# Kernel optimization log

Hardware: AMD Instinct MI355X
Metric: run time of the kernel (lower is better)

## Reference

```python
import jax, jax.numpy as jnp
import numpy as np

H = 1024   # hidden size
L = 3      # num layers
D_IN = 2048  # input size (= 2*H so every layer has the same input width)


def _bigru_layer(x_proj, W_hh, b_hh, h0):
    """Run one bidirectional GRU layer over time.
    x_proj: (T, 2, B, 3H)  input projections, time already reversed for dir=1
    W_hh:   (2, 3H, H)     hidden-to-hidden weights per direction
    b_hh:   (2, 3H)        hidden-to-hidden bias per direction
    h0:     (2, B, H)      initial hidden state per direction
    returns (T, 2, B, H)   hidden states per step (dir=1 still time-reversed)
    """
    def step(h, xp):
        # torch GRU convention: gates ordered [r, z, n]; reset gate multiplies
        # the hidden-side candidate term (W_hn h + b_hn).
        hh = jnp.einsum('dbh,dgh->dbg', h, W_hh) + b_hh[:, None, :]  # (2,B,3H)
        xr, xz, xn = jnp.split(xp, 3, axis=-1)
        hr, hz, hn = jnp.split(hh, 3, axis=-1)
        r = jax.nn.sigmoid(xr + hr)
        z = jax.nn.sigmoid(xz + hz)
        n = jnp.tanh(xn + r * hn)
        h_new = (1.0 - z) * n + z * h
        return h_new, h_new

    _, outs = jax.lax.scan(step, h0, x_proj)
    return outs


def setup_inputs() -> dict:
    key = jax.random.key(0)
    ks = jax.random.split(key, 8)
    T, B = 256, 32
    k = 1.0 / np.sqrt(H)  # torch default GRU init scale
    x = jax.random.normal(ks[0], (T, B, D_IN), dtype=jnp.float32)
    h0 = jax.random.normal(ks[1], (L * 2, B, H), dtype=jnp.float32)
    W_ih = jax.random.uniform(ks[2], (L, 2, 3 * H, D_IN), jnp.float32, -k, k)
    W_hh = jax.random.uniform(ks[3], (L, 2, 3 * H, H), jnp.float32, -k, k)
    b_ih = jax.random.uniform(ks[4], (L, 2, 3 * H), jnp.float32, -k, k)
    b_hh = jax.random.uniform(ks[5], (L, 2, 3 * H), jnp.float32, -k, k)
    return {"x": x, "h0": h0, "W_ih": W_ih, "W_hh": W_hh, "b_ih": b_ih, "b_hh": b_hh}


def reference(x, h0, W_ih, W_hh, b_ih, b_hh):
    T, B, _ = x.shape
    h0 = h0.reshape(L, 2, B, H)
    layer_input = x
    for l in range(L):
        # precompute input projections for both directions: (T, 2, B, 3H)
        xp = jnp.einsum('tbi,dgi->tdbg', layer_input, W_ih[l]) + b_ih[l][None, :, None, :]
        # reverse time for the backward direction
        xp = jnp.stack([xp[:, 0], xp[::-1, 1]], axis=1)
        outs = _bigru_layer(xp, W_hh[l], b_hh[l], h0[l])  # (T,2,B,H)
        out_f = outs[:, 0]
        out_b = outs[::-1, 1]  # un-reverse backward outputs
        layer_input = jnp.concatenate([out_f, out_b], axis=-1)  # (T,B,2H)
    return layer_input
```

## Files before the change

kernel.cpp:

```cpp
#include <hip/hip_runtime.h>
#include <hip/hip_bf16.h>
#include <stdint.h>

#define T_STEPS 256
#define BATCH   32
#define HID     1024
#define KDIM    2048
#define NDIM    6144
#define MDIM    8192

typedef __attribute__((ext_vector_type(8))) short bfrag;
typedef __attribute__((ext_vector_type(4))) float ffrag;

__device__ inline unsigned short f2bf(float f) {
  __hip_bfloat16 h = __float2bfloat16(f);
  unsigned short u;
  __builtin_memcpy(&u, &h, 2);
  return u;
}

__device__ inline void gld_lds16(const void* g, void* l) {
  __builtin_amdgcn_global_load_lds(
      (const __attribute__((address_space(1))) void*)g,
      (__attribute__((address_space(3))) void*)l,
      16, 0, 0);
}

__global__ __launch_bounds__(256) void f32_to_bf16_k(
    const float* __restrict__ src, unsigned short* __restrict__ dst, int n4) {
  int i = blockIdx.x * 256 + threadIdx.x;
  if (i >= n4) return;
  float4 v = ((const float4*)src)[i];
  ushort4 o;
  o.x = f2bf(v.x); o.y = f2bf(v.y); o.z = f2bf(v.z); o.w = f2bf(v.w);
  ((ushort4*)dst)[i] = o;
}

__global__ __launch_bounds__(256) void gemm_xp(
    const unsigned short* __restrict__ A,
    const unsigned short* __restrict__ Bw,
    const float* __restrict__ bias,
    float* __restrict__ C) {
  __shared__ __align__(16) unsigned short Asl[128 * 32];
  __shared__ __align__(16) unsigned short Bsl[128 * 32];
  const int tid  = threadIdx.x;
  const int wave = tid >> 6;
  const int lane = tid & 63;
  const int quad = lane >> 4;
  const int lm   = lane & 15;
  const int m0 = blockIdx.x * 128;
  const int n0 = blockIdx.y * 128;
  const int wm = (wave & 1) * 64;
  const int wn = (wave >> 1) * 64;

  ffrag acc[4][4];
#pragma unroll
  for (int a = 0; a < 4; a++)
#pragma unroll
    for (int b = 0; b < 4; b++) {
      ffrag z = {0.0f, 0.0f, 0.0f, 0.0f};
      acc[a][b] = z;
    }

  const int r = tid >> 2;
  const int c = tid & 3;
  const unsigned short* Ag0 = A  + (size_t)(m0 + r) * KDIM + c * 8;
  const unsigned short* Ag1 = Ag0 + (size_t)64 * KDIM;
  const unsigned short* Bg0 = Bw + (size_t)(n0 + r) * KDIM + c * 8;
  const unsigned short* Bg1 = Bg0 + (size_t)64 * KDIM;
  char* Al = (char*)Asl + wave * 1024;
  char* Bl = (char*)Bsl + wave * 1024;

  for (int kk = 0; kk < KDIM; kk += 32) {
    __syncthreads();
    gld_lds16(Ag0 + kk, Al);
    gld_lds16(Ag1 + kk, Al + 4096);
    gld_lds16(Bg0 + kk, Bl);
    gld_lds16(Bg1 + kk, Bl + 4096);
    __syncthreads();

    bfrag af[4], bf[4];
#pragma unroll
    for (int mt = 0; mt < 4; mt++)
      af[mt] = *(const bfrag*)((const char*)Asl + (wm + mt * 16 + lm) * 64 + quad * 16);
#pragma unroll
    for (int nt = 0; nt < 4; nt++)
      bf[nt] = *(const bfrag*)((const char*)Bsl + (wn + nt * 16 + lm) * 64 + quad * 16);
#pragma unroll
    for (int mt = 0; mt < 4; mt++)
#pragma unroll
      for (int nt = 0; nt < 4; nt++)
        acc[mt][nt] = __builtin_amdgcn_mfma_f32_16x16x32_bf16(
            af[mt], bf[nt], acc[mt][nt], 0, 0, 0);
  }

#pragma unroll
  for (int mt = 0; mt < 4; mt++) {
#pragma unroll
    for (int nt = 0; nt < 4; nt++) {
      int mrow = m0 + wm + mt * 16 + quad * 4;
      int ncol = n0 + wn + nt * 16 + lm;
      float bi = bias[ncol];
#pragma unroll
      for (int i = 0; i < 4; i++)
        C[(size_t)(mrow + i) * NDIM + ncol] = acc[mt][nt][i] + bi;
    }
  }
}

__device__ inline void gbar(unsigned* cnt, unsigned target) {
  __syncthreads();
  if (threadIdx.x == 0) {
    __hip_atomic_fetch_add(cnt, 1u, __ATOMIC_RELEASE, __HIP_MEMORY_SCOPE_AGENT);
    while (__hip_atomic_load(cnt, __ATOMIC_RELAXED, __HIP_MEMORY_SCOPE_AGENT) < target)
      __builtin_amdgcn_s_sleep(1);
    (void)__hip_atomic_load(cnt, __ATOMIC_ACQUIRE, __HIP_MEMORY_SCOPE_AGENT);
  }
  __syncthreads();
}

__global__ __launch_bounds__(384, 1) void gru_scan(
    const float* __restrict__ xp,
    const unsigned short* __restrict__ Wbf,
    const float* __restrict__ bhh,
    const float* __restrict__ h0,
    unsigned short* __restrict__ hbA, unsigned short* __restrict__ hbB,
    unsigned* __restrict__ bar,
    unsigned short* __restrict__ out_bf,
    float* __restrict__ out_f32) {
  __shared__ float gbuf[3][32][17];
  __shared__ float hloc[32][16];

  const int blk  = blockIdx.x;
  const int d    = blk >> 6;
  const int j0   = (blk & 63) * 16;
  const int tid  = threadIdx.x;
  const int wave = tid / 64;
  const int lane = tid & 63;
  const int quad = lane >> 4;
  const int lm   = lane & 15;
  const int g    = wave >> 1;
  const int mt   = wave & 1;

  const unsigned short* wrow =
      Wbf + ((size_t)(d * 3072 + g * 1024 + j0 + lm)) * HID + quad * 8;
  bfrag wreg[32];
#pragma unroll
  for (int kk = 0; kk < 32; kk++)
    wreg[kk] = *(const bfrag*)(wrow + kk * 32);

  const int arow_off = (d * 32 + mt * 16 + lm) * HID + quad * 8;

  for (int o = tid; o < 512; o += 384) {
    int b = o >> 4, j = o & 15;
    float v = h0[(d * 32 + b) * HID + j0 + j];
    hloc[b][j] = v;
    hbA[(d * 32 + b) * HID + j0 + j] = f2bf(v);
  }

  float bh_r[2], bh_z[2], bh_n[2];
#pragma unroll
  for (int u = 0; u < 2; u++) {
    int o = tid + u * 384;
    if (o < 512) {
      int jg = j0 + (o & 15);
      bh_r[u] = bhh[d * 3072 + jg];
      bh_z[u] = bhh[d * 3072 + 1024 + jg];
      bh_n[u] = bhh[d * 3072 + 2048 + jg];
    }
  }

  unsigned bt = 128;
  gbar(bar, bt);

  const unsigned short* hb_prev = hbA;
  unsigned short* hb_next = hbB;

  for (int s = 0; s < T_STEPS; s++) {
    const int t = d ? (T_STEPS - 1 - s) : s;

    float pxr[2], pxz[2], pxn[2];
#pragma unroll
    for (int u = 0; u < 2; u++) {
      int o = tid + u * 384;
      if (o < 512) {
        int b = o >> 4, jg = j0 + (o & 15);
        const float* xrow = xp + ((size_t)t * BATCH + b) * NDIM + d * 3072;
        pxr[u] = __builtin_nontemporal_load(xrow + jg);
        pxz[u] = __builtin_nontemporal_load(xrow + 1024 + jg);
        pxn[u] = __builtin_nontemporal_load(xrow + 2048 + jg);
      }
    }

    ffrag acc0 = {0.0f, 0.0f, 0.0f, 0.0f};
    ffrag acc1 = {0.0f, 0.0f, 0.0f, 0.0f};
    const unsigned short* ap = hb_prev + arow_off;
#pragma unroll
    for (int kk = 0; kk < 32; kk += 2) {
      bfrag a0 = *(const bfrag*)(ap + kk * 32);
      bfrag a1 = *(const bfrag*)(ap + kk * 32 + 32);
      acc0 = __builtin_amdgcn_mfma_f32_16x16x32_bf16(a0, wreg[kk],     acc0, 0, 0, 0);
      acc1 = __builtin_amdgcn_mfma_f32_16x16x32_bf16(a1, wreg[kk + 1], acc1, 0, 0, 0);
    }

    __syncthreads();
#pragma unroll
    for (int i = 0; i < 4; i++)
      gbuf[g][mt * 16 + quad * 4 + i][lm] = acc0[i] + acc1[i];
    __syncthreads();

#pragma unroll
    for (int u = 0; u < 2; u++) {
      int o = tid + u * 384;
      if (o < 512) {
        int b = o >> 4, j = o & 15;
        int jg = j0 + j;
        float hr = gbuf[0][b][j] + bh_r[u];
        float hz = gbuf[1][b][j] + bh_z[u];
        float hn = gbuf[2][b][j] + bh_n[u];
        float rr = 1.0f / (1.0f + __expf(-(pxr[u] + hr)));
        float zz = 1.0f / (1.0f + __expf(-(pxz[u] + hz)));
        float nn = tanhf(pxn[u] + rr * hn);
        float hp = hloc[b][j];
        float hv = (1.0f - zz) * nn + zz * hp;
        hloc[b][j] = hv;
        unsigned short hvb = f2bf(hv);
        hb_next[(d * 32 + b) * HID + jg] = hvb;
        size_t oi = ((size_t)t * BATCH + b) * 2048 + d * HID + jg;
        if (out_bf) __builtin_nontemporal_store(hvb, &out_bf[oi]);
        else        __builtin_nontemporal_store(hv, &out_f32[oi]);
      }
    }

    bt += 128;
    gbar(bar, bt);

    const unsigned short* tb = hb_prev;
    hb_prev = hb_next;
    hb_next = (unsigned short*)tb;
  }
}

extern "C" void kernel_launch(void* const* d_in, const int* in_sizes, int n_in,
                              void* d_out, int out_size, void* d_ws, size_t ws_size,
                              hipStream_t stream) {
  const float* x    = (const float*)d_in[0];
  const float* h0   = (const float*)d_in[1];
  const float* W_ih = (const float*)d_in[2];
  const float* W_hh = (const float*)d_in[3];
  const float* b_ih = (const float*)d_in[4];
  const float* b_hh = (const float*)d_in[5];
  float* out = (float*)d_out;

  char* w = (char*)d_ws;
  float* xp = (float*)w;                    w += (size_t)MDIM * NDIM * 4;
  unsigned short* act = (unsigned short*)w; w += (size_t)MDIM * KDIM * 2;
  unsigned short* Wub = (unsigned short*)w; w += (size_t)2 * 3072 * KDIM * 2;
  unsigned short* hbA = (unsigned short*)w; w += (size_t)2 * BATCH * HID * 2;
  unsigned short* hbB = (unsigned short*)w; w += (size_t)2 * BATCH * HID * 2;
  unsigned* bar = (unsigned*)w;             w += 256;

  hipMemsetAsync(bar, 0, 3 * sizeof(unsigned), stream);

  f32_to_bf16_k<<<16384, 256, 0, stream>>>(x, act, MDIM * KDIM / 4);

  for (int l = 0; l < 3; l++) {
    f32_to_bf16_k<<<12288, 256, 0, stream>>>(
        W_ih + (size_t)l * 2 * 3072 * KDIM, Wub, 2 * 3072 * KDIM / 4);
    dim3 gg(MDIM / 128, NDIM / 128);
    gemm_xp<<<gg, 256, 0, stream>>>(act, Wub, b_ih + l * NDIM, xp);
    f32_to_bf16_k<<<6144, 256, 0, stream>>>(
        W_hh + (size_t)l * 2 * 3072 * HID, Wub, 2 * 3072 * HID / 4);

    const float* xp_c = xp;
    const unsigned short* Wbf_c = Wub;
    const float* bhl = b_hh + l * NDIM;
    const float* h0l = h0 + (size_t)l * 2 * BATCH * HID;
    unsigned short* hbA_ = hbA; unsigned short* hbB_ = hbB;
    unsigned* bar_ = bar + l;
    unsigned short* dst_bf = (l == 2) ? nullptr : act;
    float* dst_f32 = (l == 2) ? out : nullptr;
    void* args[] = {
        (void*)&xp_c, (void*)&Wbf_c, (void*)&bhl, (void*)&h0l,
        (void*)&hbA_, (void*)&hbB_, (void*)&bar_,
        (void*)&dst_bf, (void*)&dst_f32,
    };
    hipLaunchCooperativeKernel((void*)gru_scan, dim3(128), dim3(384),
                               args, 0, stream);
  }
}
```

Measured before the change: 11.61 ms.

## Split grid barrier per direction, relax atomics, prefetch next-step projections

The single 128-block grid barrier becomes two independent 64-block barriers, one per direction, using relaxed atomics split into arrive and wait phases. The next step's input projections are loaded between arrive and wait so that load hides behind the barrier. Hidden-state reads and writes now go through relaxed agent-scope atomics, and each thread handles two packed elements in the gate stage. The recurrent weights are no longer held in registers and are reloaded from memory every step, which adds cache traffic. The removed release/acquire fences also risk memory-ordering problems.

```diff
diff --git a/kernel.cpp b/kernel.cpp
--- a/kernel.cpp
+++ b/kernel.cpp
@@ -11,6 +11,11 @@
 
 typedef __attribute__((ext_vector_type(8))) short bfrag;
 typedef __attribute__((ext_vector_type(4))) float ffrag;
+
+typedef union {
+  bfrag f;
+  unsigned long long q[2];
+} abuf;
 
 __device__ inline unsigned short f2bf(float f) {
   __hip_bfloat16 h = __float2bfloat16(f);
@@ -108,17 +113,6 @@
   }
 }
 
-__device__ inline void gbar(unsigned* cnt, unsigned target) {
-  __syncthreads();
-  if (threadIdx.x == 0) {
-    __hip_atomic_fetch_add(cnt, 1u, __ATOMIC_RELEASE, __HIP_MEMORY_SCOPE_AGENT);
-    while (__hip_atomic_load(cnt, __ATOMIC_RELAXED, __HIP_MEMORY_SCOPE_AGENT) < target)
-      __builtin_amdgcn_s_sleep(1);
-    (void)__hip_atomic_load(cnt, __ATOMIC_ACQUIRE, __HIP_MEMORY_SCOPE_AGENT);
-  }
-  __syncthreads();
-}
-
 __global__ __launch_bounds__(384, 1) void gru_scan(
     const float* __restrict__ xp,
     const unsigned short* __restrict__ Wbf,
@@ -135,43 +129,60 @@
   const int d    = blk >> 6;
   const int j0   = (blk & 63) * 16;
   const int tid  = threadIdx.x;
-  const int wave = tid / 64;
   const int lane = tid & 63;
   const int quad = lane >> 4;
   const int lm   = lane & 15;
-  const int g    = wave >> 1;
-  const int mt   = wave & 1;
+  const int g    = (tid / 64) >> 1;
+  const int mt   = (tid / 64) & 1;
+
+  unsigned* mybar = bar + d * 64;
+
+  const int gb  = tid >> 3;
+  const int gj  = (tid & 7) * 2;
+  const bool gact = (tid < 256);
+
+  if (gact) {
+    float v0 = h0[(d * 32 + gb) * HID + j0 + gj];
+    float v1 = h0[(d * 32 + gb) * HID + j0 + gj + 1];
+    hloc[gb][gj]     = v0;
+    hloc[gb][gj + 1] = v1;
+    unsigned pk = (unsigned)f2bf(v0) | ((unsigned)f2bf(v1) << 16);
+    __hip_atomic_store((unsigned*)&hbA[(d * 32 + gb) * HID + j0 + gj], pk,
+                       __ATOMIC_RELAXED, __HIP_MEMORY_SCOPE_AGENT);
+  }
+
+  float bh_r0 = 0, bh_r1 = 0, bh_z0 = 0, bh_z1 = 0, bh_n0 = 0, bh_n1 = 0;
+  if (gact) {
+    int jg = j0 + gj;
+    bh_r0 = bhh[d * 3072 + jg];        bh_r1 = bhh[d * 3072 + jg + 1];
+    bh_z0 = bhh[d * 3072 + 1024 + jg]; bh_z1 = bhh[d * 3072 + 1024 + jg + 1];
+    bh_n0 = bhh[d * 3072 + 2048 + jg]; bh_n1 = bhh[d * 3072 + 2048 + jg + 1];
+  }
 
   const unsigned short* wrow =
       Wbf + ((size_t)(d * 3072 + g * 1024 + j0 + lm)) * HID + quad * 8;
-  bfrag wreg[32];
-#pragma unroll
-  for (int kk = 0; kk < 32; kk++)
-    wreg[kk] = *(const bfrag*)(wrow + kk * 32);
-
   const int arow_off = (d * 32 + mt * 16 + lm) * HID + quad * 8;
 
-  for (int o = tid; o < 512; o += 384) {
-    int b = o >> 4, j = o & 15;
-    float v = h0[(d * 32 + b) * HID + j0 + j];
-    hloc[b][j] = v;
-    hbA[(d * 32 + b) * HID + j0 + j] = f2bf(v);
-  }
-
-  float bh_r[2], bh_z[2], bh_n[2];
-#pragma unroll
-  for (int u = 0; u < 2; u++) {
-    int o = tid + u * 384;
-    if (o < 512) {
-      int jg = j0 + (o & 15);
-      bh_r[u] = bhh[d * 3072 + jg];
-      bh_z[u] = bhh[d * 3072 + 1024 + jg];
-      bh_n[u] = bhh[d * 3072 + 2048 + jg];
-    }
-  }
-
-  unsigned bt = 128;
-  gbar(bar, bt);
+  unsigned bt = 64;
+  __syncthreads();
+  if (tid == 0)
+    __hip_atomic_fetch_add(mybar, 1u, __ATOMIC_RELAXED, __HIP_MEMORY_SCOPE_AGENT);
+
+  float2 pxr, pxz, pxn;
+  {
+    const int t0 = d ? (T_STEPS - 1) : 0;
+    const float* xrow = xp + ((size_t)t0 * BATCH + gb) * NDIM + d * 3072 + j0 + gj;
+    if (gact) {
+      pxr = *(const float2*)(xrow);
+      pxz = *(const float2*)(xrow + 1024);
+      pxn = *(const float2*)(xrow + 2048);
+    }
+  }
+  if (tid == 0) {
+    while (__hip_atomic_load(mybar, __ATOMIC_RELAXED, __HIP_MEMORY_SCOPE_AGENT) < bt)
+      __builtin_amdgcn_s_sleep(1);
+  }
+  __syncthreads();
 
   const unsigned short* hb_prev = hbA;
   unsigned short* hb_next = hbB;
@@ -179,28 +190,24 @@
   for (int s = 0; s < T_STEPS; s++) {
     const int t = d ? (T_STEPS - 1 - s) : s;
 
-    float pxr[2], pxz[2], pxn[2];
-#pragma unroll
-    for (int u = 0; u < 2; u++) {
-      int o = tid + u * 384;
-      if (o < 512) {
-        int b = o >> 4, jg = j0 + (o & 15);
-        const float* xrow = xp + ((size_t)t * BATCH + b) * NDIM + d * 3072;
-        pxr[u] = __builtin_nontemporal_load(xrow + jg);
-        pxz[u] = __builtin_nontemporal_load(xrow + 1024 + jg);
-        pxn[u] = __builtin_nontemporal_load(xrow + 2048 + jg);
-      }
+    abuf a[32];
+    const unsigned short* ap = hb_prev + arow_off;
+#pragma unroll
+    for (int kk = 0; kk < 32; kk++) {
+      a[kk].q[0] = __hip_atomic_load((const unsigned long long*)(ap + kk * 32),
+                                     __ATOMIC_RELAXED, __HIP_MEMORY_SCOPE_AGENT);
+      a[kk].q[1] = __hip_atomic_load((const unsigned long long*)(ap + kk * 32 + 4),
+                                     __ATOMIC_RELAXED, __HIP_MEMORY_SCOPE_AGENT);
     }
 
     ffrag acc0 = {0.0f, 0.0f, 0.0f, 0.0f};
     ffrag acc1 = {0.0f, 0.0f, 0.0f, 0.0f};
-    const unsigned short* ap = hb_prev + arow_off;
 #pragma unroll
     for (int kk = 0; kk < 32; kk += 2) {
-      bfrag a0 = *(const bfrag*)(ap + kk * 32);
-      bfrag a1 = *(const bfrag*)(ap + kk * 32 + 32);
-      acc0 = __builtin_amdgcn_mfma_f32_16x16x32_bf16(a0, wreg[kk],     acc0, 0, 0, 0);
-      acc1 = __builtin_amdgcn_mfma_f32_16x16x32_bf16(a1, wreg[kk + 1], acc1, 0, 0, 0);
+      bfrag w0 = *(const bfrag*)(wrow + kk * 32);
+      bfrag w1 = *(const bfrag*)(wrow + (kk + 1) * 32);
+      acc0 = __builtin_amdgcn_mfma_f32_16x16x32_bf16(a[kk].f,     w0, acc0, 0, 0, 0);
+      acc1 = __builtin_amdgcn_mfma_f32_16x16x32_bf16(a[kk + 1].f, w1, acc1, 0, 0, 0);
     }
 
     __syncthreads();
@@ -209,31 +216,53 @@
       gbuf[g][mt * 16 + quad * 4 + i][lm] = acc0[i] + acc1[i];
     __syncthreads();
 
-#pragma unroll
-    for (int u = 0; u < 2; u++) {
-      int o = tid + u * 384;
-      if (o < 512) {
-        int b = o >> 4, j = o & 15;
-        int jg = j0 + j;
-        float hr = gbuf[0][b][j] + bh_r[u];
-        float hz = gbuf[1][b][j] + bh_z[u];
-        float hn = gbuf[2][b][j] + bh_n[u];
-        float rr = 1.0f / (1.0f + __expf(-(pxr[u] + hr)));
-        float zz = 1.0f / (1.0f + __expf(-(pxz[u] + hz)));
-        float nn = tanhf(pxn[u] + rr * hn);
-        float hp = hloc[b][j];
-        float hv = (1.0f - zz) * nn + zz * hp;
-        hloc[b][j] = hv;
-        unsigned short hvb = f2bf(hv);
-        hb_next[(d * 32 + b) * HID + jg] = hvb;
-        size_t oi = ((size_t)t * BATCH + b) * 2048 + d * HID + jg;
-        if (out_bf) __builtin_nontemporal_store(hvb, &out_bf[oi]);
-        else        __builtin_nontemporal_store(hv, &out_f32[oi]);
+    if (gact) {
+      int jg = j0 + gj;
+      float hr0 = gbuf[0][gb][gj]     + bh_r0;
+      float hr1 = gbuf[0][gb][gj + 1] + bh_r1;
+      float hz0 = gbuf[1][gb][gj]     + bh_z0;
+      float hz1 = gbuf[1][gb][gj + 1] + bh_z1;
+      float hn0 = gbuf[2][gb][gj]     + bh_n0;
+      float hn1 = gbuf[2][gb][gj + 1] + bh_n1;
+      float rr0 = 1.0f / (1.0f + __expf(-(pxr.x + hr0)));
+      float rr1 = 1.0f / (1.0f + __expf(-(pxr.y + hr1)));
+      float zz0 = 1.0f / (1.0f + __expf(-(pxz.x + hz0)));
+      float zz1 = 1.0f / (1.0f + __expf(-(pxz.y + hz1)));
+      float nn0 = tanhf(pxn.x + rr0 * hn0);
+      float nn1 = tanhf(pxn.y + rr1 * hn1);
+      float hv0 = (1.0f - zz0) * nn0 + zz0 * hloc[gb][gj];
+      float hv1 = (1.0f - zz1) * nn1 + zz1 * hloc[gb][gj + 1];
+      hloc[gb][gj]     = hv0;
+      hloc[gb][gj + 1] = hv1;
+      unsigned pk = (unsigned)f2bf(hv0) | ((unsigned)f2bf(hv1) << 16);
+      __hip_atomic_store((unsigned*)&hb_next[(d * 32 + gb) * HID + jg], pk,
+                         __ATOMIC_RELAXED, __HIP_MEMORY_SCOPE_AGENT);
+      size_t oi = ((size_t)t * BATCH + gb) * 2048 + d * HID + jg;
+      if (out_bf) {
+        *(unsigned*)&out_bf[oi] = pk;
+      } else {
+        float2 ov; ov.x = hv0; ov.y = hv1;
+        *(float2*)&out_f32[oi] = ov;
       }
     }
 
-    bt += 128;
-    gbar(bar, bt);
+    bt += 64;
+    __syncthreads();
+    if (tid == 0)
+      __hip_atomic_fetch_add(mybar, 1u, __ATOMIC_RELAXED, __HIP_MEMORY_SCOPE_AGENT);
+    if (gact) {
+      int s2 = (s + 1 < T_STEPS) ? s + 1 : s;
+      int t2 = d ? (T_STEPS - 1 - s2) : s2;
+      const float* xrow = xp + ((size_t)t2 * BATCH + gb) * NDIM + d * 3072 + j0 + gj;
+      pxr = *(const float2*)(xrow);
+      pxz = *(const float2*)(xrow + 1024);
+      pxn = *(const float2*)(xrow + 2048);
+    }
+    if (tid == 0) {
+      while (__hip_atomic_load(mybar, __ATOMIC_RELAXED, __HIP_MEMORY_SCOPE_AGENT) < bt)
+        __builtin_amdgcn_s_sleep(1);
+    }
+    __syncthreads();
 
     const unsigned short* tb = hb_prev;
     hb_prev = hb_next;
@@ -258,9 +287,9 @@
   unsigned short* Wub = (unsigned short*)w; w += (size_t)2 * 3072 * KDIM * 2;
   unsigned short* hbA = (unsigned short*)w; w += (size_t)2 * BATCH * HID * 2;
   unsigned short* hbB = (unsigned short*)w; w += (size_t)2 * BATCH * HID * 2;
-  unsigned* bar = (unsigned*)w;             w += 256;
-
-  hipMemsetAsync(bar, 0, 3 * sizeof(unsigned), stream);
+  unsigned* bar = (unsigned*)w;             w += 3 * 2 * 256;
+
+  hipMemsetAsync(bar, 0, 3 * 2 * 256, stream);
 
   f32_to_bf16_k<<<16384, 256, 0, stream>>>(x, act, MDIM * KDIM / 4);
 
@@ -277,7 +306,7 @@
     const float* bhl = b_hh + l * NDIM;
     const float* h0l = h0 + (size_t)l * 2 * BATCH * HID;
     unsigned short* hbA_ = hbA; unsigned short* hbB_ = hbB;
-    unsigned* bar_ = bar + l;
+    unsigned* bar_ = bar + l * 128;
     unsigned short* dst_bf = (l == 2) ? nullptr : act;
     float* dst_f32 = (l == 2) ? out : nullptr;
     void* args[] = {
```

Result: faster. 10.70 ms (-7.9%).
